# Performance work log

Hardware: AMD Instinct MI355X
Metric: run time of the kernel (lower is better)

## Reference

```python
import jax, jax.numpy as jnp
import numpy as np
from jax import lax

T, B, INPUT_DIM, RNN_DIM = 512, 64, 512, 512
STDV = 1.0 / np.sqrt(float(RNN_DIM))


def setup_inputs() -> dict:
    key = jax.random.key(0)
    k0, k1, k2, k3 = jax.random.split(key, 4)
    input_vectors = jax.random.normal(k0, (T, B, INPUT_DIM), dtype=jnp.float32)
    # params mimic reset_parameters: uniform(-stdv, stdv), stdv = 1/sqrt(rnn_dim)
    weight = jax.random.uniform(k1, (INPUT_DIM + RNN_DIM, RNN_DIM), dtype=jnp.float32, minval=-STDV, maxval=STDV)
    bias = jax.random.uniform(k2, (1, RNN_DIM), dtype=jnp.float32, minval=-STDV, maxval=STDV)
    init_hidden = jax.random.uniform(k3, (1, RNN_DIM), dtype=jnp.float32, minval=-STDV, maxval=STDV)
    return {"input_vectors": input_vectors, "weight": weight, "bias": bias, "init_hidden": init_hidden}


def reference(input_vectors, weight, bias, init_hidden):
    # direction='l'. Output at step i is the hidden state BEFORE the i-th update
    # (the torch code appends prev_hidden before computing new_hidden).
    batch = input_vectors.shape[1]
    rnn_dim = init_hidden.shape[1]
    h0 = jnp.broadcast_to(init_hidden, (batch, rnn_dim))

    def step(h, x):  # h: [B, R], x: [B, D]
        new_h = jnp.tanh(jnp.concatenate([x, h], axis=1) @ weight + bias)
        return new_h, h  # emit pre-update hidden, carry post-update

    _, seq_hidden = lax.scan(step, h0, input_vectors)  # [T, B, R]
    return seq_hidden
```

## Files before the change

### kernel.cpp

```cpp
#include <hip/hip_runtime.h>
#include <hip/hip_bf16.h>
#include <hip/hip_fp16.h>

#define T_STEPS 512
#define BATCH   64
#define DIM     512
#define TOT_PAIRS 256
#define REG_PAIRS 160
#define LDS_PAIRS 64
#define STR_PAIRS 32

typedef _Float16 half2_t __attribute__((ext_vector_type(2)));
typedef _Float16 half8_t __attribute__((ext_vector_type(8)));
typedef short    bf16x8 __attribute__((ext_vector_type(8)));
typedef float    f32x4  __attribute__((ext_vector_type(4)));

static __device__ __forceinline__ unsigned short f2bf(float f) {
    union { float f; unsigned u; } v; v.f = f;
    unsigned r = v.u + 0x7fffu + ((v.u >> 16) & 1u);
    return (unsigned short)(r >> 16);
}

static __device__ __forceinline__ float fast_tanh(float x) {
    float e = __expf(2.0f * x);
    return 1.0f - 2.0f * __builtin_amdgcn_rcpf(e + 1.0f);
}

__global__ __launch_bounds__(256) void tr_cvt_kernel(const float* __restrict__ src,
                                                     unsigned short* __restrict__ dst) {
    __shared__ float tile[32][33];
    const int bx = blockIdx.x * 32;
    const int by = blockIdx.y * 32;
    const int tx = threadIdx.x;
    const int ty = threadIdx.y;
    #pragma unroll
    for (int i = ty; i < 32; i += 8)
        tile[i][tx] = src[(size_t)(by + i) * DIM + (bx + tx)];
    __syncthreads();
    #pragma unroll
    for (int i = ty; i < 32; i += 8)
        dst[(size_t)(bx + i) * DIM + (by + tx)] = f2bf(tile[tx][i]);
}

__global__ __launch_bounds__(256) void pack_wh_kernel(const float* __restrict__ W,
                                                      half2_t* __restrict__ WhP) {
    const int gid = blockIdx.x * 256 + threadIdx.x;
    const int p = gid >> 9, jj = gid & 511;
    float lo = W[(size_t)(512 + 2 * p) * DIM + jj];
    float hi = W[(size_t)(512 + 2 * p + 1) * DIM + jj];
    half2_t v; v[0] = (_Float16)lo; v[1] = (_Float16)hi;
    WhP[gid] = v;
}

__global__ __launch_bounds__(256) void gemm_z_kernel(const float* __restrict__ X,
                                                     const unsigned short* __restrict__ WxT,
                                                     const float* __restrict__ bias,
                                                     _Float16* __restrict__ Zo) {
    const int bm   = blockIdx.y;
    const int bn   = blockIdx.x;
    const int wave = threadIdx.x >> 6;
    const int lane = threadIdx.x & 63;
    const int mBase = bm * 128 + (wave >> 1) * 64;
    const int nBase = bn * 128 + (wave & 1) * 64;
    const int l15 = lane & 15;
    const int q   = lane >> 4;
    f32x4 acc[4][4] = {};
    for (int kt = 0; kt < 512; kt += 32) {
        const int kk = kt + q * 8;
        bf16x8 a[4], b[4];
        #pragma unroll
        for (int i = 0; i < 4; ++i) {
            const float* ap = X + (size_t)(mBase + i * 16 + l15) * DIM + kk;
            float4 f0 = *(const float4*)(ap);
            float4 f1 = *(const float4*)(ap + 4);
            bf16x8 av;
            av[0] = (short)f2bf(f0.x); av[1] = (short)f2bf(f0.y);
            av[2] = (short)f2bf(f0.z); av[3] = (short)f2bf(f0.w);
            av[4] = (short)f2bf(f1.x); av[5] = (short)f2bf(f1.y);
            av[6] = (short)f2bf(f1.z); av[7] = (short)f2bf(f1.w);
            a[i] = av;
        }
        #pragma unroll
        for (int i = 0; i < 4; ++i)
            b[i] = *(const bf16x8*)(WxT + (size_t)(nBase + i * 16 + l15) * DIM + kk);
        #pragma unroll
        for (int mi = 0; mi < 4; ++mi)
            #pragma unroll
            for (int ni = 0; ni < 4; ++ni)
                acc[mi][ni] = __builtin_amdgcn_mfma_f32_16x16x32_bf16(a[mi], b[ni], acc[mi][ni], 0, 0, 0);
    }
    #pragma unroll
    for (int ni = 0; ni < 4; ++ni) {
        const int col = nBase + ni * 16 + l15;
        const float bv = bias[col];
        #pragma unroll
        for (int mi = 0; mi < 4; ++mi) {
            #pragma unroll
            for (int rg = 0; rg < 4; ++rg) {
                const int row = mBase + mi * 16 + q * 4 + rg;
                Zo[(size_t)row * DIM + col] = (_Float16)(acc[mi][ni][rg] + bv);
            }
        }
    }
}

__global__ __launch_bounds__(512, 2) void rnn_rec_kernel(const _Float16* __restrict__ Z,
                                                         const half2_t* __restrict__ WhP,
                                                         const float* __restrict__ h0,
                                                         float* __restrict__ out) {
    __shared__ half8_t wlds4[(LDS_PAIRS / 4) * DIM];
    __shared__ _Float16 hsh[2][DIM];
    const int r = blockIdx.x;
    const int j = threadIdx.x;

    #pragma unroll
    for (int g = 0; g < LDS_PAIRS / 4; ++g) {
        half2_t p0 = WhP[(size_t)(REG_PAIRS + 4 * g + 0) * DIM + j];
        half2_t p1 = WhP[(size_t)(REG_PAIRS + 4 * g + 1) * DIM + j];
        half2_t p2 = WhP[(size_t)(REG_PAIRS + 4 * g + 2) * DIM + j];
        half2_t p3 = WhP[(size_t)(REG_PAIRS + 4 * g + 3) * DIM + j];
        half8_t v;
        v[0] = p0[0]; v[1] = p0[1]; v[2] = p1[0]; v[3] = p1[1];
        v[4] = p2[0]; v[5] = p2[1]; v[6] = p3[0]; v[7] = p3[1];
        wlds4[g * DIM + j] = v;
    }
    half2_t w[REG_PAIRS];
    #pragma unroll
    for (int p = 0; p < REG_PAIRS; ++p) w[p] = WhP[(size_t)p * DIM + j];
    #pragma unroll
    for (int p = 0; p < REG_PAIRS; ++p) asm volatile("" : "+v"(w[p]));

    float h = h0[j];
    out[(size_t)r * DIM + j] = h;
    hsh[0][j] = (_Float16)h;
    __syncthreads();

    float zv = (float)Z[(size_t)r * DIM + j];

    for (int t = 0; t < T_STEPS - 1; ++t) {
        float zn = (float)Z[((size_t)(t + 1) * BATCH + r) * DIM + j];
        half2_t sw0[16];
        #pragma unroll
        for (int p = 0; p < 16; ++p)
            sw0[p] = WhP[(size_t)(REG_PAIRS + LDS_PAIRS + p) * DIM + j];

        const half8_t* h8 = (const half8_t*)&hsh[t & 1][0];
        float a0 = zv, a1 = 0.f, a2 = 0.f, a3 = 0.f;
        #pragma unroll
        for (int c = 0; c < REG_PAIRS / 4; ++c) {
            half8_t hv = h8[c];
            a0 = __builtin_amdgcn_fdot2(w[4*c+0], __builtin_shufflevector(hv, hv, 0, 1), a0, false);
            a1 = __builtin_amdgcn_fdot2(w[4*c+1], __builtin_shufflevector(hv, hv, 2, 3), a1, false);
            a2 = __builtin_amdgcn_fdot2(w[4*c+2], __builtin_shufflevector(hv, hv, 4, 5), a2, false);
            a3 = __builtin_amdgcn_fdot2(w[4*c+3], __builtin_shufflevector(hv, hv, 6, 7), a3, false);
        }
        half2_t sw1[16];
        #pragma unroll
        for (int p = 0; p < 16; ++p)
            sw1[p] = WhP[(size_t)(REG_PAIRS + LDS_PAIRS + 16 + p) * DIM + j];
        #pragma unroll
        for (int g = 0; g < LDS_PAIRS / 4; ++g) {
            half8_t hv = h8[REG_PAIRS / 4 + g];
            half8_t wv = wlds4[g * DIM + j];
            a0 = __builtin_amdgcn_fdot2(__builtin_shufflevector(wv, wv, 0, 1), __builtin_shufflevector(hv, hv, 0, 1), a0, false);
            a1 = __builtin_amdgcn_fdot2(__builtin_shufflevector(wv, wv, 2, 3), __builtin_shufflevector(hv, hv, 2, 3), a1, false);
            a2 = __builtin_amdgcn_fdot2(__builtin_shufflevector(wv, wv, 4, 5), __builtin_shufflevector(hv, hv, 4, 5), a2, false);
            a3 = __builtin_amdgcn_fdot2(__builtin_shufflevector(wv, wv, 6, 7), __builtin_shufflevector(hv, hv, 6, 7), a3, false);
        }
        #pragma unroll
        for (int c = 0; c < 4; ++c) {
            half8_t hv = h8[(REG_PAIRS + LDS_PAIRS) / 4 + c];
            a0 = __builtin_amdgcn_fdot2(sw0[4*c+0], __builtin_shufflevector(hv, hv, 0, 1), a0, false);
            a1 = __builtin_amdgcn_fdot2(sw0[4*c+1], __builtin_shufflevector(hv, hv, 2, 3), a1, false);
            a2 = __builtin_amdgcn_fdot2(sw0[4*c+2], __builtin_shufflevector(hv, hv, 4, 5), a2, false);
            a3 = __builtin_amdgcn_fdot2(sw0[4*c+3], __builtin_shufflevector(hv, hv, 6, 7), a3, false);
        }
        #pragma unroll
        for (int c = 0; c < 4; ++c) {
            half8_t hv = h8[(REG_PAIRS + LDS_PAIRS) / 4 + 4 + c];
            a0 = __builtin_amdgcn_fdot2(sw1[4*c+0], __builtin_shufflevector(hv, hv, 0, 1), a0, false);
            a1 = __builtin_amdgcn_fdot2(sw1[4*c+1], __builtin_shufflevector(hv, hv, 2, 3), a1, false);
            a2 = __builtin_amdgcn_fdot2(sw1[4*c+2], __builtin_shufflevector(hv, hv, 4, 5), a2, false);
            a3 = __builtin_amdgcn_fdot2(sw1[4*c+3], __builtin_shufflevector(hv, hv, 6, 7), a3, false);
        }
        float hn = fast_tanh((a0 + a1) + (a2 + a3));
        out[((size_t)(t + 1) * BATCH + r) * DIM + j] = hn;
        hsh[(t + 1) & 1][j] = (_Float16)hn;
        zv = zn;
        asm volatile("s_waitcnt lgkmcnt(0)\n\ts_barrier" ::: "memory");
    }
}

extern "C" void kernel_launch(void* const* d_in, const int* in_sizes, int n_in,
                              void* d_out, int out_size, void* d_ws, size_t ws_size,
                              hipStream_t stream) {
    const float* X    = (const float*)d_in[0];
    const float* W    = (const float*)d_in[1];
    const float* bias = (const float*)d_in[2];
    const float* h0   = (const float*)d_in[3];
    float* out = (float*)d_out;

    char* ws = (char*)d_ws;
    unsigned short* WxT = (unsigned short*)(ws);
    half2_t*        WhP = (half2_t*)(ws + 524288);
    _Float16*       Zh  = (_Float16*)(ws + 1048576);

    dim3 tb(32, 8);
    tr_cvt_kernel<<<dim3(16, 16), tb, 0, stream>>>(W, WxT);
    pack_wh_kernel<<<512, 256, 0, stream>>>(W, WhP);
    gemm_z_kernel<<<dim3(4, 256), 256, 0, stream>>>(X, WxT, bias, Zh);
    rnn_rec_kernel<<<64, 512, 0, stream>>>(Zh, WhP, h0, out);
}
```

Baseline: 1.116 ms.

## Split recurrent dot product across two half-waves with xor-shuffle reduction

The recurrence kernel now launches 1024 threads per batch row instead of 512. Each output column's 256-pair K reduction is split between the two 32-lane halves of a wavefront, and the partial sums are combined with a cross-lane xor shuffle. The per-thread register, LDS and streamed weight slices are halved, which shortens each thread's serial dot-product chain per time step. The cost is an extra shuffle per step, a 1024-thread barrier, and half the lanes idling during the output and hidden-state writes.

```diff
diff --git a/kernel.cpp b/kernel.cpp
--- a/kernel.cpp
+++ b/kernel.cpp
@@ -5,10 +5,9 @@
 #define T_STEPS 512
 #define BATCH   64
 #define DIM     512
-#define TOT_PAIRS 256
-#define REG_PAIRS 160
-#define LDS_PAIRS 64
-#define STR_PAIRS 32
+#define REG_PAIRS 80
+#define LDS_PAIRS 32
+#define STR_PAIRS 16
 
 typedef _Float16 half2_t __attribute__((ext_vector_type(2)));
 typedef _Float16 half8_t __attribute__((ext_vector_type(8)));
@@ -104,47 +103,56 @@
     }
 }
 
-__global__ __launch_bounds__(512, 2) void rnn_rec_kernel(const _Float16* __restrict__ Z,
-                                                         const half2_t* __restrict__ WhP,
-                                                         const float* __restrict__ h0,
-                                                         float* __restrict__ out) {
-    __shared__ half8_t wlds4[(LDS_PAIRS / 4) * DIM];
+__global__ __launch_bounds__(1024, 4) void rnn_rec_kernel(const _Float16* __restrict__ Z,
+                                                          const half2_t* __restrict__ WhP,
+                                                          const float* __restrict__ h0,
+                                                          float* __restrict__ out) {
+    __shared__ half8_t wlds4[(LDS_PAIRS / 4) * 1024];
     __shared__ _Float16 hsh[2][DIM];
-    const int r = blockIdx.x;
-    const int j = threadIdx.x;
+    const int r   = blockIdx.x;
+    const int tid = threadIdx.x;
+    const int l   = tid & 63;
+    const int wv  = tid >> 6;
+    const int j   = (wv << 5) | (l & 31);
+    const int kh  = l >> 5;
+
+    const half2_t* Wcol = WhP + (size_t)(kh * 128) * DIM + j;
 
     #pragma unroll
     for (int g = 0; g < LDS_PAIRS / 4; ++g) {
-        half2_t p0 = WhP[(size_t)(REG_PAIRS + 4 * g + 0) * DIM + j];
-        half2_t p1 = WhP[(size_t)(REG_PAIRS + 4 * g + 1) * DIM + j];
-        half2_t p2 = WhP[(size_t)(REG_PAIRS + 4 * g + 2) * DIM + j];
-        half2_t p3 = WhP[(size_t)(REG_PAIRS + 4 * g + 3) * DIM + j];
+        half2_t p0 = Wcol[(size_t)(REG_PAIRS + 4 * g + 0) * DIM];
+        half2_t p1 = Wcol[(size_t)(REG_PAIRS + 4 * g + 1) * DIM];
+        half2_t p2 = Wcol[(size_t)(REG_PAIRS + 4 * g + 2) * DIM];
+        half2_t p3 = Wcol[(size_t)(REG_PAIRS + 4 * g + 3) * DIM];
         half8_t v;
         v[0] = p0[0]; v[1] = p0[1]; v[2] = p1[0]; v[3] = p1[1];
         v[4] = p2[0]; v[5] = p2[1]; v[6] = p3[0]; v[7] = p3[1];
-        wlds4[g * DIM + j] = v;
+        wlds4[g * 1024 + tid] = v;
     }
     half2_t w[REG_PAIRS];
     #pragma unroll
-    for (int p = 0; p < REG_PAIRS; ++p) w[p] = WhP[(size_t)p * DIM + j];
+    for (int p = 0; p < REG_PAIRS; ++p) w[p] = Wcol[(size_t)p * DIM];
     #pragma unroll
     for (int p = 0; p < REG_PAIRS; ++p) asm volatile("" : "+v"(w[p]));
 
     float h = h0[j];
-    out[(size_t)r * DIM + j] = h;
-    hsh[0][j] = (_Float16)h;
+    if (kh == 0) {
+        out[(size_t)r * DIM + j] = h;
+        hsh[0][j] = (_Float16)h;
+    }
     __syncthreads();
 
-    float zv = (float)Z[(size_t)r * DIM + j];
+    float zv = (kh == 0) ? (float)Z[(size_t)r * DIM + j] : 0.0f;
 
     for (int t = 0; t < T_STEPS - 1; ++t) {
-        float zn = (float)Z[((size_t)(t + 1) * BATCH + r) * DIM + j];
-        half2_t sw0[16];
-        #pragma unroll
-        for (int p = 0; p < 16; ++p)
-            sw0[p] = WhP[(size_t)(REG_PAIRS + LDS_PAIRS + p) * DIM + j];
-
-        const half8_t* h8 = (const half8_t*)&hsh[t & 1][0];
+        float zn = 0.0f;
+        if (kh == 0) zn = (float)Z[((size_t)(t + 1) * BATCH + r) * DIM + j];
+        half2_t sw0[8];
+        #pragma unroll
+        for (int p = 0; p < 8; ++p)
+            sw0[p] = Wcol[(size_t)(REG_PAIRS + LDS_PAIRS + p) * DIM];
+
+        const half8_t* h8 = (const half8_t*)&hsh[t & 1][0] + (kh << 5);
         float a0 = zv, a1 = 0.f, a2 = 0.f, a3 = 0.f;
         #pragma unroll
         for (int c = 0; c < REG_PAIRS / 4; ++c) {
@@ -154,21 +162,21 @@
             a2 = __builtin_amdgcn_fdot2(w[4*c+2], __builtin_shufflevector(hv, hv, 4, 5), a2, false);
             a3 = __builtin_amdgcn_fdot2(w[4*c+3], __builtin_shufflevector(hv, hv, 6, 7), a3, false);
         }
-        half2_t sw1[16];
-        #pragma unroll
-        for (int p = 0; p < 16; ++p)
-            sw1[p] = WhP[(size_t)(REG_PAIRS + LDS_PAIRS + 16 + p) * DIM + j];
+        half2_t sw1[8];
+        #pragma unroll
+        for (int p = 0; p < 8; ++p)
+            sw1[p] = Wcol[(size_t)(REG_PAIRS + LDS_PAIRS + 8 + p) * DIM];
         #pragma unroll
         for (int g = 0; g < LDS_PAIRS / 4; ++g) {
             half8_t hv = h8[REG_PAIRS / 4 + g];
-            half8_t wv = wlds4[g * DIM + j];
-            a0 = __builtin_amdgcn_fdot2(__builtin_shufflevector(wv, wv, 0, 1), __builtin_shufflevector(hv, hv, 0, 1), a0, false);
-            a1 = __builtin_amdgcn_fdot2(__builtin_shufflevector(wv, wv, 2, 3), __builtin_shufflevector(hv, hv, 2, 3), a1, false);
-            a2 = __builtin_amdgcn_fdot2(__builtin_shufflevector(wv, wv, 4, 5), __builtin_shufflevector(hv, hv, 4, 5), a2, false);
-            a3 = __builtin_amdgcn_fdot2(__builtin_shufflevector(wv, wv, 6, 7), __builtin_shufflevector(hv, hv, 6, 7), a3, false);
-        }
-        #pragma unroll
-        for (int c = 0; c < 4; ++c) {
+            half8_t wv8 = wlds4[g * 1024 + tid];
+            a0 = __builtin_amdgcn_fdot2(__builtin_shufflevector(wv8, wv8, 0, 1), __builtin_shufflevector(hv, hv, 0, 1), a0, false);
+            a1 = __builtin_amdgcn_fdot2(__builtin_shufflevector(wv8, wv8, 2, 3), __builtin_shufflevector(hv, hv, 2, 3), a1, false);
+            a2 = __builtin_amdgcn_fdot2(__builtin_shufflevector(wv8, wv8, 4, 5), __builtin_shufflevector(hv, hv, 4, 5), a2, false);
+            a3 = __builtin_amdgcn_fdot2(__builtin_shufflevector(wv8, wv8, 6, 7), __builtin_shufflevector(hv, hv, 6, 7), a3, false);
+        }
+        #pragma unroll
+        for (int c = 0; c < 2; ++c) {
             half8_t hv = h8[(REG_PAIRS + LDS_PAIRS) / 4 + c];
             a0 = __builtin_amdgcn_fdot2(sw0[4*c+0], __builtin_shufflevector(hv, hv, 0, 1), a0, false);
             a1 = __builtin_amdgcn_fdot2(sw0[4*c+1], __builtin_shufflevector(hv, hv, 2, 3), a1, false);
@@ -176,16 +184,20 @@
             a3 = __builtin_amdgcn_fdot2(sw0[4*c+3], __builtin_shufflevector(hv, hv, 6, 7), a3, false);
         }
         #pragma unroll
-        for (int c = 0; c < 4; ++c) {
-            half8_t hv = h8[(REG_PAIRS + LDS_PAIRS) / 4 + 4 + c];
+        for (int c = 0; c < 2; ++c) {
+            half8_t hv = h8[(REG_PAIRS + LDS_PAIRS) / 4 + 2 + c];
             a0 = __builtin_amdgcn_fdot2(sw1[4*c+0], __builtin_shufflevector(hv, hv, 0, 1), a0, false);
             a1 = __builtin_amdgcn_fdot2(sw1[4*c+1], __builtin_shufflevector(hv, hv, 2, 3), a1, false);
             a2 = __builtin_amdgcn_fdot2(sw1[4*c+2], __builtin_shufflevector(hv, hv, 4, 5), a2, false);
             a3 = __builtin_amdgcn_fdot2(sw1[4*c+3], __builtin_shufflevector(hv, hv, 6, 7), a3, false);
         }
-        float hn = fast_tanh((a0 + a1) + (a2 + a3));
-        out[((size_t)(t + 1) * BATCH + r) * DIM + j] = hn;
-        hsh[(t + 1) & 1][j] = (_Float16)hn;
+        float s = (a0 + a1) + (a2 + a3);
+        s += __shfl_xor(s, 32, 64);
+        float hn = fast_tanh(s);
+        if (kh == 0) {
+            out[((size_t)(t + 1) * BATCH + r) * DIM + j] = hn;
+            hsh[(t + 1) & 1][j] = (_Float16)hn;
+        }
         zv = zn;
         asm volatile("s_waitcnt lgkmcnt(0)\n\ts_barrier" ::: "memory");
     }
@@ -209,5 +221,5 @@
     tr_cvt_kernel<<<dim3(16, 16), tb, 0, stream>>>(W, WxT);
     pack_wh_kernel<<<512, 256, 0, stream>>>(W, WhP);
     gemm_z_kernel<<<dim3(4, 256), 256, 0, stream>>>(X, WxT, bias, Zh);
-    rnn_rec_kernel<<<64, 512, 0, stream>>>(Zh, WhP, h0, out);
-}
+    rnn_rec_kernel<<<64, 1024, 0, stream>>>(Zh, WhP, h0, out);
+}
```

Measured after the change: 1.101 ms. About the same (-1.4%).

## Replace per-batch fdot2 recurrence with MFMA recurrence over 16-row batch tiles

Applied to the files above, without the earlier changes.

The recurrent step is recast as a 16x512 by 512x512 matrix product on MFMA f16 instructions, with each block handling 16 batch rows, so only 4 blocks run instead of 64. Wh is stored transposed in f16, partly held in registers and partly in LDS, and the input projection Z is written in a fragment-matched layout so each lane loads its accumulator seeds directly. This replaces the scalar dot-product work and weight streaming per step with matrix-core work, but uses far fewer CUs and adds a second barrier per step.

```diff
diff --git a/kernel.cpp b/kernel.cpp
--- a/kernel.cpp
+++ b/kernel.cpp
@@ -5,10 +5,7 @@
 #define T_STEPS 512
 #define BATCH   64
 #define DIM     512
-#define TOT_PAIRS 256
-#define REG_PAIRS 160
-#define LDS_PAIRS 64
-#define STR_PAIRS 32
+#define ROWS    16
 
 typedef _Float16 half2_t __attribute__((ext_vector_type(2)));
 typedef _Float16 half8_t __attribute__((ext_vector_type(8)));
@@ -42,14 +39,20 @@
         dst[(size_t)(bx + i) * DIM + (by + tx)] = f2bf(tile[tx][i]);
 }
 
-__global__ __launch_bounds__(256) void pack_wh_kernel(const float* __restrict__ W,
-                                                      half2_t* __restrict__ WhP) {
-    const int gid = blockIdx.x * 256 + threadIdx.x;
-    const int p = gid >> 9, jj = gid & 511;
-    float lo = W[(size_t)(512 + 2 * p) * DIM + jj];
-    float hi = W[(size_t)(512 + 2 * p + 1) * DIM + jj];
-    half2_t v; v[0] = (_Float16)lo; v[1] = (_Float16)hi;
-    WhP[gid] = v;
+__global__ __launch_bounds__(256) void tr_cvt_f16_kernel(const float* __restrict__ src,
+                                                         _Float16* __restrict__ dst) {
+    __shared__ float tile[32][33];
+    const int bx = blockIdx.x * 32;
+    const int by = blockIdx.y * 32;
+    const int tx = threadIdx.x;
+    const int ty = threadIdx.y;
+    #pragma unroll
+    for (int i = ty; i < 32; i += 8)
+        tile[i][tx] = src[(size_t)(by + i) * DIM + (bx + tx)];
+    __syncthreads();
+    #pragma unroll
+    for (int i = ty; i < 32; i += 8)
+        dst[(size_t)(bx + i) * DIM + (by + tx)] = (_Float16)tile[tx][i];
 }
 
 __global__ __launch_bounds__(256) void gemm_z_kernel(const float* __restrict__ X,
@@ -93,101 +96,115 @@
     for (int ni = 0; ni < 4; ++ni) {
         const int col = nBase + ni * 16 + l15;
         const float bv = bias[col];
+        const int w_ = col >> 6, ct_ = (col >> 4) & 3, l15_ = col & 15;
         #pragma unroll
         for (int mi = 0; mi < 4; ++mi) {
             #pragma unroll
             for (int rg = 0; rg < 4; ++rg) {
                 const int row = mBase + mi * 16 + q * 4 + rg;
-                Zo[(size_t)row * DIM + col] = (_Float16)(acc[mi][ni][rg] + bv);
+                const int t_ = row >> 6, brow = row & 63;
+                const int b_ = brow >> 4, r4 = brow & 15;
+                const int l_ = (r4 >> 2) * 16 + l15_;
+                const int i_ = ct_ * 4 + (r4 & 3);
+                Zo[(size_t)t_ * 32768 + (size_t)((b_ * 8 + w_) * 64 + l_) * 16 + i_] =
+                    (_Float16)(acc[mi][ni][rg] + bv);
             }
         }
     }
 }
 
-__global__ __launch_bounds__(512, 2) void rnn_rec_kernel(const _Float16* __restrict__ Z,
-                                                         const half2_t* __restrict__ WhP,
-                                                         const float* __restrict__ h0,
-                                                         float* __restrict__ out) {
-    __shared__ half8_t wlds4[(LDS_PAIRS / 4) * DIM];
-    __shared__ _Float16 hsh[2][DIM];
-    const int r = blockIdx.x;
-    const int j = threadIdx.x;
-
-    #pragma unroll
-    for (int g = 0; g < LDS_PAIRS / 4; ++g) {
-        half2_t p0 = WhP[(size_t)(REG_PAIRS + 4 * g + 0) * DIM + j];
-        half2_t p1 = WhP[(size_t)(REG_PAIRS + 4 * g + 1) * DIM + j];
-        half2_t p2 = WhP[(size_t)(REG_PAIRS + 4 * g + 2) * DIM + j];
-        half2_t p3 = WhP[(size_t)(REG_PAIRS + 4 * g + 3) * DIM + j];
-        half8_t v;
-        v[0] = p0[0]; v[1] = p0[1]; v[2] = p1[0]; v[3] = p1[1];
-        v[4] = p2[0]; v[5] = p2[1]; v[6] = p3[0]; v[7] = p3[1];
-        wlds4[g * DIM + j] = v;
-    }
-    half2_t w[REG_PAIRS];
-    #pragma unroll
-    for (int p = 0; p < REG_PAIRS; ++p) w[p] = WhP[(size_t)p * DIM + j];
-    #pragma unroll
-    for (int p = 0; p < REG_PAIRS; ++p) asm volatile("" : "+v"(w[p]));
-
-    float h = h0[j];
-    out[(size_t)r * DIM + j] = h;
-    hsh[0][j] = (_Float16)h;
+__global__ __launch_bounds__(512, 2) void rnn_mfma_kernel(const _Float16* __restrict__ Zw,
+                                                          const _Float16* __restrict__ WhT,
+                                                          const float* __restrict__ h0,
+                                                          float* __restrict__ out) {
+    __shared__ _Float16 WlA[65536];
+    __shared__ _Float16 Ah[8192];
+    const int tid = threadIdx.x;
+    const int w = tid >> 6, l = tid & 63;
+    const int l15 = l & 15, q = l >> 4;
+    const int b = blockIdx.x;
+    const int wbase = w * 64;
+
+    half8_t bw[12][4];
+    #pragma unroll
+    for (int kt = 0; kt < 12; ++kt)
+        #pragma unroll
+        for (int ct = 0; ct < 4; ++ct)
+            bw[kt][ct] = *(const half8_t*)(WhT + (size_t)(wbase + ct * 16 + l15) * DIM + kt * 32 + q * 8);
+    #pragma unroll
+    for (int kt = 0; kt < 12; ++kt)
+        #pragma unroll
+        for (int ct = 0; ct < 4; ++ct)
+            asm volatile("" : "+v"(bw[kt][ct]));
+    #pragma unroll
+    for (int ktl = 0; ktl < 4; ++ktl)
+        #pragma unroll
+        for (int ct = 0; ct < 4; ++ct) {
+            half8_t v = *(const half8_t*)(WhT + (size_t)(wbase + ct * 16 + l15) * DIM + (12 + ktl) * 32 + q * 8);
+            *(half8_t*)(WlA + (size_t)((w * 16 + ct * 4 + ktl) * 512 + l * 8)) = v;
+        }
+
+    const int hi = l15 >> 3, l7 = l15 & 7;
+    const int abase = w * 1024 + hi * 32 + q * 8 + l7;
+    float* p0 = out + (size_t)(b * 16 + q * 4) * DIM + wbase + l15;
+    float h0c[4];
+    #pragma unroll
+    for (int ct = 0; ct < 4; ++ct) h0c[ct] = h0[wbase + ct * 16 + l15];
+    #pragma unroll
+    for (int ct = 0; ct < 4; ++ct)
+        #pragma unroll
+        for (int rg = 0; rg < 4; ++rg) {
+            p0[rg * DIM + ct * 16] = h0c[ct];
+            Ah[abase + (ct >> 1) * 512 + (ct & 1) * 64 + rg * 128] = (_Float16)h0c[ct];
+        }
     __syncthreads();
 
-    float zv = (float)Z[(size_t)r * DIM + j];
+    const int aslot = (l & 3) * 128 + (l >> 2) * 8;
+    const _Float16* pz = Zw + ((size_t)(b * 8 + w) * 64 + l) * 16;
+    half8_t z0 = *(const half8_t*)(pz);
+    half8_t z1 = *(const half8_t*)(pz + 8);
+    float* pout = out + (size_t)(BATCH + b * 16 + q * 4) * DIM + wbase + l15;
 
     for (int t = 0; t < T_STEPS - 1; ++t) {
-        float zn = (float)Z[((size_t)(t + 1) * BATCH + r) * DIM + j];
-        half2_t sw0[16];
-        #pragma unroll
-        for (int p = 0; p < 16; ++p)
-            sw0[p] = WhP[(size_t)(REG_PAIRS + LDS_PAIRS + p) * DIM + j];
-
-        const half8_t* h8 = (const half8_t*)&hsh[t & 1][0];
-        float a0 = zv, a1 = 0.f, a2 = 0.f, a3 = 0.f;
-        #pragma unroll
-        for (int c = 0; c < REG_PAIRS / 4; ++c) {
-            half8_t hv = h8[c];
-            a0 = __builtin_amdgcn_fdot2(w[4*c+0], __builtin_shufflevector(hv, hv, 0, 1), a0, false);
-            a1 = __builtin_amdgcn_fdot2(w[4*c+1], __builtin_shufflevector(hv, hv, 2, 3), a1, false);
-            a2 = __builtin_amdgcn_fdot2(w[4*c+2], __builtin_shufflevector(hv, hv, 4, 5), a2, false);
-            a3 = __builtin_amdgcn_fdot2(w[4*c+3], __builtin_shufflevector(hv, hv, 6, 7), a3, false);
-        }
-        half2_t sw1[16];
-        #pragma unroll
-        for (int p = 0; p < 16; ++p)
-            sw1[p] = WhP[(size_t)(REG_PAIRS + LDS_PAIRS + 16 + p) * DIM + j];
-        #pragma unroll
-        for (int g = 0; g < LDS_PAIRS / 4; ++g) {
-            half8_t hv = h8[REG_PAIRS / 4 + g];
-            half8_t wv = wlds4[g * DIM + j];
-            a0 = __builtin_amdgcn_fdot2(__builtin_shufflevector(wv, wv, 0, 1), __builtin_shufflevector(hv, hv, 0, 1), a0, false);
-            a1 = __builtin_amdgcn_fdot2(__builtin_shufflevector(wv, wv, 2, 3), __builtin_shufflevector(hv, hv, 2, 3), a1, false);
-            a2 = __builtin_amdgcn_fdot2(__builtin_shufflevector(wv, wv, 4, 5), __builtin_shufflevector(hv, hv, 4, 5), a2, false);
-            a3 = __builtin_amdgcn_fdot2(__builtin_shufflevector(wv, wv, 6, 7), __builtin_shufflevector(hv, hv, 6, 7), a3, false);
-        }
-        #pragma unroll
-        for (int c = 0; c < 4; ++c) {
-            half8_t hv = h8[(REG_PAIRS + LDS_PAIRS) / 4 + c];
-            a0 = __builtin_amdgcn_fdot2(sw0[4*c+0], __builtin_shufflevector(hv, hv, 0, 1), a0, false);
-            a1 = __builtin_amdgcn_fdot2(sw0[4*c+1], __builtin_shufflevector(hv, hv, 2, 3), a1, false);
-            a2 = __builtin_amdgcn_fdot2(sw0[4*c+2], __builtin_shufflevector(hv, hv, 4, 5), a2, false);
-            a3 = __builtin_amdgcn_fdot2(sw0[4*c+3], __builtin_shufflevector(hv, hv, 6, 7), a3, false);
-        }
-        #pragma unroll
-        for (int c = 0; c < 4; ++c) {
-            half8_t hv = h8[(REG_PAIRS + LDS_PAIRS) / 4 + 4 + c];
-            a0 = __builtin_amdgcn_fdot2(sw1[4*c+0], __builtin_shufflevector(hv, hv, 0, 1), a0, false);
-            a1 = __builtin_amdgcn_fdot2(sw1[4*c+1], __builtin_shufflevector(hv, hv, 2, 3), a1, false);
-            a2 = __builtin_amdgcn_fdot2(sw1[4*c+2], __builtin_shufflevector(hv, hv, 4, 5), a2, false);
-            a3 = __builtin_amdgcn_fdot2(sw1[4*c+3], __builtin_shufflevector(hv, hv, 6, 7), a3, false);
-        }
-        float hn = fast_tanh((a0 + a1) + (a2 + a3));
-        out[((size_t)(t + 1) * BATCH + r) * DIM + j] = hn;
-        hsh[(t + 1) & 1][j] = (_Float16)hn;
-        zv = zn;
+        f32x4 acc[4];
+        #pragma unroll
+        for (int ct = 0; ct < 4; ++ct)
+            #pragma unroll
+            for (int rg = 0; rg < 4; ++rg) {
+                const int i = ct * 4 + rg;
+                acc[ct][rg] = (float)(i < 8 ? z0[i] : z1[i - 8]);
+            }
+        half8_t zn0 = *(const half8_t*)(pz + (size_t)(t + 1) * 32768);
+        half8_t zn1 = *(const half8_t*)(pz + (size_t)(t + 1) * 32768 + 8);
+
+        #pragma unroll
+        for (int kt = 0; kt < 12; ++kt) {
+            half8_t af = *(const half8_t*)(Ah + kt * 512 + aslot);
+            #pragma unroll
+            for (int ct = 0; ct < 4; ++ct)
+                acc[ct] = __builtin_amdgcn_mfma_f32_16x16x32_f16(af, bw[kt][ct], acc[ct], 0, 0, 0);
+        }
+        #pragma unroll
+        for (int ktl = 0; ktl < 4; ++ktl) {
+            half8_t af = *(const half8_t*)(Ah + (12 + ktl) * 512 + aslot);
+            #pragma unroll
+            for (int ct = 0; ct < 4; ++ct) {
+                half8_t wf = *(const half8_t*)(WlA + (size_t)((w * 16 + ct * 4 + ktl) * 512 + l * 8));
+                acc[ct] = __builtin_amdgcn_mfma_f32_16x16x32_f16(af, wf, acc[ct], 0, 0, 0);
+            }
+        }
         asm volatile("s_waitcnt lgkmcnt(0)\n\ts_barrier" ::: "memory");
+        #pragma unroll
+        for (int ct = 0; ct < 4; ++ct)
+            #pragma unroll
+            for (int rg = 0; rg < 4; ++rg) {
+                const float hv = fast_tanh(acc[ct][rg]);
+                pout[rg * DIM + ct * 16] = hv;
+                Ah[abase + (ct >> 1) * 512 + (ct & 1) * 64 + rg * 128] = (_Float16)hv;
+            }
+        asm volatile("s_waitcnt lgkmcnt(0)\n\ts_barrier" ::: "memory");
+        pout += BATCH * DIM;
+        z0 = zn0; z1 = zn1;
     }
 }
 
@@ -202,12 +219,12 @@
 
     char* ws = (char*)d_ws;
     unsigned short* WxT = (unsigned short*)(ws);
-    half2_t*        WhP = (half2_t*)(ws + 524288);
-    _Float16*       Zh  = (_Float16*)(ws + 1048576);
+    _Float16*       WhT = (_Float16*)(ws + 524288);
+    _Float16*       Zws = (_Float16*)(ws + 1048576);
 
     dim3 tb(32, 8);
     tr_cvt_kernel<<<dim3(16, 16), tb, 0, stream>>>(W, WxT);
-    pack_wh_kernel<<<512, 256, 0, stream>>>(W, WhP);
-    gemm_z_kernel<<<dim3(4, 256), 256, 0, stream>>>(X, WxT, bias, Zh);
-    rnn_rec_kernel<<<64, 512, 0, stream>>>(Zh, WhP, h0, out);
-}
+    tr_cvt_f16_kernel<<<dim3(16, 16), tb, 0, stream>>>(W + 512 * 512, WhT);
+    gemm_z_kernel<<<dim3(4, 256), 256, 0, stream>>>(X, WxT, bias, Zws);
+    rnn_mfma_kernel<<<4, 512, 0, stream>>>(Zws, WhT, h0, out);
+}
```

Measured after the change: 1.197 ms. +7.2%, slower.
